# Performance work log

Measured on AMD Instinct MI355X. Metric: run time of the kernel, lower is better.

Reference implementation:

```python
import jax, jax.numpy as jnp
import numpy as np

V, E, G = 25000, 50000, 1024
D_IN, E_IN, D, EH = 74, 12, 64, 128
STEPS, S2S, L, NT = 6, 6, 3, 1


def setup_inputs() -> dict:
    key = jax.random.key(0)
    ks = jax.random.split(key, 20)
    p = lambda k, shp: (jax.random.normal(k, shp, jnp.float32) * 0.05)
    return {
        "node_feats": jax.random.normal(ks[0], (V, D_IN), jnp.float32),
        "edge_feats": jax.random.normal(ks[1], (E, E_IN), jnp.float32),
        "src": jax.random.randint(ks[2], (E,), 0, V),
        "dst": jax.random.randint(ks[3], (E,), 0, V),
        "node2graph": jnp.sort(jax.random.randint(ks[4], (V,), 0, G)),
        "W_proj": p(ks[5], (D_IN, D)), "b_proj": jnp.zeros((D,), jnp.float32),
        "W_e1": p(ks[6], (E_IN, EH)), "b_e1": jnp.zeros((EH,), jnp.float32),
        "W_e2": p(ks[7], (EH, D * D)), "b_e2": jnp.zeros((D * D,), jnp.float32),
        "b_conv": jnp.zeros((D,), jnp.float32),
        "gru_W_ih": p(ks[8], (3 * D, D)), "gru_W_hh": p(ks[9], (3 * D, D)),
        "gru_b_ih": jnp.zeros((3 * D,), jnp.float32), "gru_b_hh": jnp.zeros((3 * D,), jnp.float32),
        "lstm_W_ih0": p(ks[10], (4 * D, 2 * D)), "lstm_W_hh0": p(ks[11], (4 * D, D)),
        "lstm_b_ih0": jnp.zeros((4 * D,), jnp.float32), "lstm_b_hh0": jnp.zeros((4 * D,), jnp.float32),
        "lstm_W_ih_r": p(ks[12], (L - 1, 4 * D, D)), "lstm_W_hh_r": p(ks[13], (L - 1, 4 * D, D)),
        "lstm_b_ih_r": jnp.zeros((L - 1, 4 * D), jnp.float32), "lstm_b_hh_r": jnp.zeros((L - 1, 4 * D), jnp.float32),
        "W1": p(ks[14], (2 * D, D)), "b1": jnp.zeros((D,), jnp.float32),
        "bn_gamma": jnp.ones((D,), jnp.float32), "bn_beta": jnp.zeros((D,), jnp.float32),
        "bn_mean": jnp.zeros((D,), jnp.float32), "bn_var": jnp.ones((D,), jnp.float32),
        "W2": p(ks[15], (D, 4 * NT)), "b2": jnp.zeros((4 * NT,), jnp.float32),
    }


def reference(node_feats, edge_feats, src, dst, node2graph,
              W_proj, b_proj, W_e1, b_e1, W_e2, b_e2, b_conv,
              gru_W_ih, gru_W_hh, gru_b_ih, gru_b_hh,
              lstm_W_ih0, lstm_W_hh0, lstm_b_ih0, lstm_b_hh0,
              lstm_W_ih_r, lstm_W_hh_r, lstm_b_ih_r, lstm_b_hh_r,
              W1, b1, bn_gamma, bn_beta, bn_mean, bn_var, W2, b2):
    # --- MPNNGNN: project + ReLU, then NNConv(sum) + ReLU + GRU, x STEPS ---
    h = jax.nn.relu(node_feats @ W_proj + b_proj)                       # (V, D)
    # edge network: per-edge (D,D) mixing matrix (edge_feats constant across steps)
    We = (jax.nn.relu(edge_feats @ W_e1 + b_e1) @ W_e2 + b_e2).reshape(E, D, D)

    def mp_step(hh, _):
        m = jnp.einsum('ed,edo->eo', hh[src], We)                       # per-edge message
        agg = jax.ops.segment_sum(m, dst, num_segments=V) + b_conv      # NNConv sum + bias
        x = jax.nn.relu(agg)
        gi = x @ gru_W_ih.T + gru_b_ih                                  # GRU (torch gate order r,z,n)
        gh = hh @ gru_W_hh.T + gru_b_hh
        ir, iz, inn = jnp.split(gi, 3, axis=-1)
        hr, hz, hn = jnp.split(gh, 3, axis=-1)
        r = jax.nn.sigmoid(ir + hr)
        z = jax.nn.sigmoid(iz + hz)
        n = jnp.tanh(inn + r * hn)
        return (1.0 - z) * n + z * hh, None

    h, _ = jax.lax.scan(mp_step, h, None, length=STEPS)

    # --- Set2Set readout ---
    q_star = jnp.zeros((G, 2 * D), h.dtype)
    hs = jnp.zeros((L, G, D), h.dtype)
    cs = jnp.zeros((L, G, D), h.dtype)
    for _ in range(S2S):
        x = q_star
        nh, nc = [], []
        for l in range(L):                                              # stacked LSTM, seq len 1
            Wih = lstm_W_ih0 if l == 0 else lstm_W_ih_r[l - 1]
            Whh = lstm_W_hh0 if l == 0 else lstm_W_hh_r[l - 1]
            bih = lstm_b_ih0 if l == 0 else lstm_b_ih_r[l - 1]
            bhh = lstm_b_hh0 if l == 0 else lstm_b_hh_r[l - 1]
            gates = x @ Wih.T + bih + hs[l] @ Whh.T + bhh               # torch order i,f,g,o
            i, f, g, o = jnp.split(gates, 4, axis=-1)
            c = jax.nn.sigmoid(f) * cs[l] + jax.nn.sigmoid(i) * jnp.tanh(g)
            hc = jax.nn.sigmoid(o) * jnp.tanh(c)
            nh.append(hc); nc.append(c)
            x = hc
        hs, cs = jnp.stack(nh), jnp.stack(nc)
        q = x                                                           # (G, D)
        e = jnp.sum(h * q[node2graph], axis=-1)                         # (V,) attention logits
        emax = jax.lax.stop_gradient(jax.ops.segment_max(e, node2graph, num_segments=G))
        emax = jnp.where(jnp.isfinite(emax), emax, 0.0)
        ez = jnp.exp(e - emax[node2graph])                              # per-graph softmax
        denom = jax.ops.segment_sum(ez, node2graph, num_segments=G)
        alpha = ez / jnp.maximum(denom[node2graph], 1e-12)
        readout = jax.ops.segment_sum(h * alpha[:, None], node2graph, num_segments=G)
        q_star = jnp.concatenate([q, readout], axis=-1)                 # (G, 2D)

    # --- evidential head: Linear + ReLU + BatchNorm(eval) + Linear ---
    h1 = jax.nn.relu(q_star @ W1 + b1)
    hbn = bn_gamma * (h1 - bn_mean) * jax.lax.rsqrt(bn_var + 1e-5) + bn_beta
    out = hbn @ W2 + b2                                                 # (G, 4*NT)
    means, logl, loga, logb = jnp.split(out, 4, axis=1)
    MINV = 1e-6
    lam = jax.nn.softplus(logl) + MINV
    alp = jax.nn.softplus(loga) + MINV + 1.0
    bet = jax.nn.softplus(logb) + MINV
    return jnp.stack([means, lam, alp, bet], axis=2).reshape(out.shape)
```

## Files before the change

kernel.cpp:

```cpp
#include <hip/hip_runtime.h>
#include <stdint.h>

#define V_N 25000
#define E_N 50000
#define G_N 1024
#define DIN 74
#define EIN 12
#define NSTEPS 6
#define NS2S 6
#define MPAD 50048

typedef unsigned int u32;
typedef unsigned short u16;
typedef __attribute__((ext_vector_type(8))) short bf16x8v;
typedef __attribute__((ext_vector_type(4))) float f32x4v;

typedef __attribute__((address_space(3))) void lds_void;
typedef __attribute__((address_space(1))) void gbl_void;

__device__ __forceinline__ void gload_lds16(const void* g, void* l) {
  __builtin_amdgcn_global_load_lds((gbl_void*)g, (lds_void*)l, 16, 0, 0);
}

__device__ __forceinline__ u16 f2bf(float f) {
  u32 u = __float_as_uint(f);
  u = (u + 0x7fffu + ((u >> 16) & 1u)) >> 16;
  return (u16)u;
}
__device__ __forceinline__ u32 pack2bf(float lo, float hi) {
  return (u32)f2bf(lo) | ((u32)f2bf(hi) << 16);
}
__device__ __forceinline__ float bflo(u32 w){ return __uint_as_float(w << 16); }
__device__ __forceinline__ float bfhi(u32 w){ return __uint_as_float(w & 0xffff0000u); }
__device__ __forceinline__ float sigf(float x){ return 1.f/(1.f + expf(-x)); }
__device__ __forceinline__ float splusf(float x){ return fmaxf(x, 0.f) + log1pf(expf(-fabsf(x))); }

__global__ void prep_kernel(const float* gWih, const float* gWhh,
                            const float* lWih0, const float* lWhh0,
                            const float* lWihr, const float* lWhhr,
                            const float* We2,
                            float* gWihT, float* gWhhT,
                            u32* TW40, u32* TU40, u32* TW4r, u32* TU4r,
                            u16* WbT) {
  int idx = blockIdx.x * 256 + threadIdx.x;
  if (idx < 12288) { int d = idx / 192, r = idx % 192; gWihT[idx] = gWih[r*64 + d]; return; }
  idx -= 12288;
  if (idx < 12288) { int d = idx / 192, r = idx % 192; gWhhT[idx] = gWhh[r*64 + d]; return; }
  idx -= 12288;
  if (idx < 16384) { int q = idx >> 2, j = idx & 3; int k8 = q >> 8, r = q & 255;
                     TW40[idx] = pack2bf(lWih0[r*128 + k8*8 + 2*j], lWih0[r*128 + k8*8 + 2*j + 1]); return; }
  idx -= 16384;
  if (idx < 8192)  { int q = idx >> 2, j = idx & 3; int k8 = q >> 8, r = q & 255;
                     TU40[idx] = pack2bf(lWhh0[r*64 + k8*8 + 2*j], lWhh0[r*64 + k8*8 + 2*j + 1]); return; }
  idx -= 8192;
  if (idx < 16384) { int l = idx >> 13, rem = idx & 8191; int q = rem >> 2, j = rem & 3;
                     int k8 = q >> 8, r = q & 255;
                     TW4r[idx] = pack2bf(lWihr[l*16384 + r*64 + k8*8 + 2*j],
                                         lWihr[l*16384 + r*64 + k8*8 + 2*j + 1]); return; }
  idx -= 16384;
  if (idx < 16384) { int l = idx >> 13, rem = idx & 8191; int q = rem >> 2, j = rem & 3;
                     int k8 = q >> 8, r = q & 255;
                     TU4r[idx] = pack2bf(lWhhr[l*16384 + r*64 + k8*8 + 2*j],
                                         lWhhr[l*16384 + r*64 + k8*8 + 2*j + 1]); return; }
  idx -= 16384;
  { int n = idx / 128, k = idx % 128; WbT[idx] = f2bf(We2[k*4096 + n]); }
}

__global__ void proj_kernel(const float* nf, const float* Wp, const float* bp, float* h) {
  int v = blockIdx.x * 4 + (threadIdx.x >> 6);
  int o = threadIdx.x & 63;
  if (v >= V_N) return;
  float acc = bp[o];
  const float* row = nf + (size_t)v * DIN;
  #pragma unroll 2
  for (int d = 0; d < DIN; ++d) acc += row[d] * Wp[d*64 + o];
  h[(size_t)v*64 + o] = fmaxf(acc, 0.f);
}

__global__ void edgenet_kernel(const float* ef, const float* W1, const float* b1, u16* zb) {
  int e = blockIdx.x * 2 + (threadIdx.x >> 7);
  int k = threadIdx.x & 127;
  float acc = 0.f;
  if (e < E_N) {
    acc = b1[k];
    const float* row = ef + (size_t)e * EIN;
    #pragma unroll
    for (int i = 0; i < EIN; ++i) acc += row[i] * W1[i*128 + k];
    acc = fmaxf(acc, 0.f);
  }
  zb[(size_t)e*128 + k] = f2bf(acc);
}

__global__ __launch_bounds__(512) void fusedmsg_kernel(const u16* zb, const u16* WbT, const float* be2,
                                                       const float* h, const int* src, const int* dst,
                                                       float* agg) {
  __shared__ __align__(16) u16 As[16384];
  __shared__ __align__(16) u16 Bs[2][16384];
  __shared__ float hS[128][66];
  int t = threadIdx.x;
  int e0 = blockIdx.x * 128;

  for (int it = 0; it < 16; ++it) {
    int idx = it * 512 + t;
    int el = idx >> 6, d = idx & 63;
    int e = e0 + el;
    int sv = (e < E_N) ? src[e] : 0;
    hS[el][d] = h[(size_t)sv * 64 + d];
  }
  {
    const char* Ag = (const char*)(zb + (size_t)e0 * 128);
    char* Al = (char*)As;
    #pragma unroll
    for (int it = 0; it < 4; ++it) {
      int f = it * 512 + t;
      int r = f >> 4, s = f & 15;
      int gc = s ^ (r & 7);
      gload_lds16(Ag + r*256 + gc*16, Al + (size_t)(f & ~63) * 16);
    }
  }
  {
    const char* Bg = (const char*)WbT;
    char* Bl = (char*)Bs[0];
    #pragma unroll
    for (int it = 0; it < 4; ++it) {
      int f = it * 512 + t;
      int r = f >> 4, s = f & 15;
      int gc = s ^ (r & 7);
      gload_lds16(Bg + r*256 + gc*16, Bl + (size_t)(f & ~63) * 16);
    }
  }
  __syncthreads();

  int w = t >> 6, lane = t & 63;
  int wr = w >> 1, wc = w & 1;
  float macc[2][4][4];
  #pragma unroll
  for (int mi = 0; mi < 2; ++mi)
    #pragma unroll
    for (int ni = 0; ni < 4; ++ni)
      #pragma unroll
      for (int r = 0; r < 4; ++r) macc[mi][ni][r] = 0.f;

  for (int nt = 0; nt < 32; ++nt) {
    int buf = nt & 1;
    if (nt < 31) {
      const char* Bg = (const char*)(WbT + (size_t)(nt + 1) * 128 * 128);
      char* Bl = (char*)Bs[buf ^ 1];
      #pragma unroll
      for (int it = 0; it < 4; ++it) {
        int f = it * 512 + t;
        int r = f >> 4, s = f & 15;
        int gc = s ^ (r & 7);
        gload_lds16(Bg + r*256 + gc*16, Bl + (size_t)(f & ~63) * 16);
      }
    }
    f32x4v acc[2][4];
    #pragma unroll
    for (int ni = 0; ni < 4; ++ni) {
      float b = be2[nt*128 + wc*64 + ni*16 + (lane & 15)];
      #pragma unroll
      for (int mi = 0; mi < 2; ++mi) acc[mi][ni] = (f32x4v){b, b, b, b};
    }
    const char* Ab = (const char*)As;
    const char* Bb = (const char*)Bs[buf];
    #pragma unroll
    for (int ks = 0; ks < 4; ++ks) {
      int cb = ks * 4 + (lane >> 4);
      bf16x8v af[2], bf[4];
      #pragma unroll
      for (int mi = 0; mi < 2; ++mi) {
        int arow = wr*32 + mi*16 + (lane & 15);
        af[mi] = *(const bf16x8v*)(Ab + arow*256 + ((cb ^ (arow & 7)) << 4));
      }
      #pragma unroll
      for (int ni = 0; ni < 4; ++ni) {
        int brow = wc*64 + ni*16 + (lane & 15);
        bf[ni] = *(const bf16x8v*)(Bb + brow*256 + ((cb ^ (brow & 7)) << 4));
      }
      #pragma unroll
      for (int mi = 0; mi < 2; ++mi)
        #pragma unroll
        for (int ni = 0; ni < 4; ++ni)
          acc[mi][ni] = __builtin_amdgcn_mfma_f32_16x16x32_bf16(af[mi], bf[ni], acc[mi][ni], 0, 0, 0);
    }
    int d0 = 2*nt + wc;
    #pragma unroll
    for (int mi = 0; mi < 2; ++mi)
      #pragma unroll
      for (int r = 0; r < 4; ++r) {
        int row = wr*32 + mi*16 + ((lane >> 4) << 2) + r;
        float hv = hS[row][d0];
        #pragma unroll
        for (int ni = 0; ni < 4; ++ni)
          macc[mi][ni][r] += hv * acc[mi][ni][r];
      }
    __syncthreads();
  }

  float* red = (float*)Bs;
  __syncthreads();
  if (wc == 1) {
    #pragma unroll
    for (int mi = 0; mi < 2; ++mi)
      #pragma unroll
      for (int ni = 0; ni < 4; ++ni)
        #pragma unroll
        for (int r = 0; r < 4; ++r)
          red[((wr*64 + lane)*32) + (mi*4 + ni)*4 + r] = macc[mi][ni][r];
  }
  __syncthreads();
  if (wc == 0) {
    #pragma unroll
    for (int mi = 0; mi < 2; ++mi)
      #pragma unroll
      for (int r = 0; r < 4; ++r) {
        int row = wr*32 + mi*16 + ((lane >> 4) << 2) + r;
        int e = e0 + row;
        if (e < E_N) {
          int dv = dst[e];
          #pragma unroll
          for (int ni = 0; ni < 4; ++ni) {
            float val = macc[mi][ni][r] + red[((wr*64 + lane)*32) + (mi*4 + ni)*4 + r];
            atomicAdd(&agg[(size_t)dv*64 + ni*16 + (lane & 15)], val);
          }
        }
      }
  }
}

__global__ void gru_kernel(const float* aggc, const float* bconv, const float* WihT, const float* WhhT,
                           const float* bih, const float* bhh, float* h, float* aggz) {
  int wbase = (blockIdx.x * 4 + (threadIdx.x >> 6)) * 4;
  int o = threadIdx.x & 63;
  float xv[4], hv[4];
  #pragma unroll
  for (int n = 0; n < 4; ++n) {
    int v = wbase + n;
    if (v < V_N) { xv[n] = fmaxf(aggc[(size_t)v*64 + o] + bconv[o], 0.f); hv[n] = h[(size_t)v*64 + o]; }
    else { xv[n] = 0.f; hv[n] = 0.f; }
  }
  float ar[4] = {0,0,0,0}, az[4] = {0,0,0,0}, an[4] = {0,0,0,0};
  float br[4] = {0,0,0,0}, bz[4] = {0,0,0,0}, bn2[4] = {0,0,0,0};
  #pragma unroll 4
  for (int d = 0; d < 64; ++d) {
    float wr = WihT[d*192 + o], wz = WihT[d*192 + 64 + o], wn = WihT[d*192 + 128 + o];
    float ur = WhhT[d*192 + o], uz = WhhT[d*192 + 64 + o], un = WhhT[d*192 + 128 + o];
    #pragma unroll
    for (int n = 0; n < 4; ++n) {
      float xd = __shfl(xv[n], d);
      float hd = __shfl(hv[n], d);
      ar[n] += xd*wr; az[n] += xd*wz; an[n] += xd*wn;
      br[n] += hd*ur; bz[n] += hd*uz; bn2[n] += hd*un;
    }
  }
  float b_r = bih[o] + bhh[o], b_z = bih[64+o] + bhh[64+o];
  float bin = bih[128+o], bhn = bhh[128+o];
  #pragma unroll
  for (int n = 0; n < 4; ++n) {
    int v = wbase + n;
    if (v >= V_N) continue;
    float r  = sigf(ar[n] + br[n] + b_r);
    float z  = sigf(az[n] + bz[n] + b_z);
    float nn = tanhf(an[n] + bin + r*(bn2[n] + bhn));
    h[(size_t)v*64 + o] = (1.f - z)*nn + z*hv[n];
    aggz[(size_t)v*64 + o] = 0.f;
  }
}

__global__ void gstart_kernel(const int* n2g, int* gstart) {
  int g = blockIdx.x * 256 + threadIdx.x;
  if (g > G_N) return;
  int lo = 0, hi = V_N;
  while (lo < hi) { int mid = (lo + hi) >> 1; if (n2g[mid] < g) lo = mid + 1; else hi = mid; }
  gstart[g] = lo;
}

__global__ __launch_bounds__(256) void s2s_kernel(const float* h, const int* gstart,
    const uint4* TW40, const uint4* TU40, const uint4* TW4r, const uint4* TU4r,
    const float* bih0, const float* bhh0, const float* bihr, const float* bhhr,
    float* qstar) {
  __shared__ float sq[4][128];
  __shared__ float sx[4][128];
  __shared__ float shs[4][3][64], scs[4][3][64];
  __shared__ float sg[4][256];
  int tt = threadIdx.x;
  int g0blk = blockIdx.x * 4;
  int w = tt >> 6, lane = tt & 63;
  int nstart = gstart[g0blk + w], nend = gstart[g0blk + w + 1];

  for (int i = tt; i < 512; i += 256) ((float*)sq)[i] = 0.f;
  for (int i = tt; i < 768; i += 256) { ((float*)shs)[i] = 0.f; ((float*)scs)[i] = 0.f; }
  __syncthreads();

  for (int iter = 0; iter < NS2S; ++iter) {
    for (int i = tt; i < 512; i += 256) ((float*)sx)[i] = ((float*)sq)[i];
    __syncthreads();

    for (int l = 0; l < 3; ++l) {
      const uint4* TW = (l == 0) ? TW40 : TW4r + (size_t)(l-1) * 2048;
      const uint4* TU = (l == 0) ? TU40 : TU4r + (size_t)(l-1) * 2048;
      const float* bi = (l == 0) ? bih0 : bihr + (l-1)*256;
      const float* bh = (l == 0) ? bhh0 : bhhr + (l-1)*256;
      float bsum = bi[tt] + bh[tt];
      float acc[4] = {bsum, bsum, bsum, bsum};
      if (l == 0) {
        #pragma unroll
        for (int k8 = 0; k8 < 16; ++k8) {
          uint4 u = TW[k8*256 + tt];
          #pragma unroll
          for (int gi = 0; gi < 4; ++gi) {
            const float4 xa = *(const float4*)&sx[gi][k8*8];
            const float4 xb = *(const float4*)&sx[gi][k8*8 + 4];
            acc[gi] += xa.x*bflo(u.x) + xa.y*bfhi(u.x) + xa.z*bflo(u.y) + xa.w*bfhi(u.y)
                     + xb.x*bflo(u.z) + xb.y*bfhi(u.z) + xb.z*bflo(u.w) + xb.w*bfhi(u.w);
          }
        }
      } else {
        #pragma unroll
        for (int k8 = 0; k8 < 8; ++k8) {
          uint4 u = TW[k8*256 + tt];
          #pragma unroll
          for (int gi = 0; gi < 4; ++gi) {
            const float4 xa = *(const float4*)&sx[gi][k8*8];
            const float4 xb = *(const float4*)&sx[gi][k8*8 + 4];
            acc[gi] += xa.x*bflo(u.x) + xa.y*bfhi(u.x) + xa.z*bflo(u.y) + xa.w*bfhi(u.y)
                     + xb.x*bflo(u.z) + xb.y*bfhi(u.z) + xb.z*bflo(u.w) + xb.w*bfhi(u.w);
          }
        }
      }
      #pragma unroll
      for (int k8 = 0; k8 < 8; ++k8) {
        uint4 u = TU[k8*256 + tt];
        #pragma unroll
        for (int gi = 0; gi < 4; ++gi) {
          const float4 ha = *(const float4*)&shs[gi][l][k8*8];
          const float4 hb = *(const float4*)&shs[gi][l][k8*8 + 4];
          acc[gi] += ha.x*bflo(u.x) + ha.y*bfhi(u.x) + ha.z*bflo(u.y) + ha.w*bfhi(u.y)
                   + hb.x*bflo(u.z) + hb.y*bfhi(u.z) + hb.z*bflo(u.w) + hb.w*bfhi(u.w);
        }
      }
      #pragma unroll
      for (int gi = 0; gi < 4; ++gi) sg[gi][tt] = acc[gi];
      __syncthreads();
      {
        int gq = tt >> 6, r = tt & 63;
        float gv_i = sg[gq][r], gv_f = sg[gq][64+r], gv_g = sg[gq][128+r], gv_o = sg[gq][192+r];
        float c = sigf(gv_f)*scs[gq][l][r] + sigf(gv_i)*tanhf(gv_g);
        float hc = sigf(gv_o)*tanhf(c);
        scs[gq][l][r] = c; shs[gq][l][r] = hc; sx[gq][r] = hc;
      }
      __syncthreads();
    }

    {
      float q_l = sx[w][lane];
      float lmax = -3.4e38f;
      int i = nstart;
      for (; i + 1 < nend; i += 2) {
        float h0 = h[(size_t)i*64 + lane];
        float h1 = h[(size_t)(i+1)*64 + lane];
        float v0 = h0 * q_l, v1 = h1 * q_l;
        #pragma unroll
        for (int off = 32; off; off >>= 1) { v0 += __shfl_xor(v0, off); v1 += __shfl_xor(v1, off); }
        lmax = fmaxf(lmax, fmaxf(v0, v1));
      }
      if (i < nend) {
        float h0 = h[(size_t)i*64 + lane];
        float v0 = h0 * q_l;
        #pragma unroll
        for (int off = 32; off; off >>= 1) v0 += __shfl_xor(v0, off);
        lmax = fmaxf(lmax, v0);
      }
      float lsum = 0.f, accv = 0.f;
      i = nstart;
      for (; i + 1 < nend; i += 2) {
        float h0 = h[(size_t)i*64 + lane];
        float h1 = h[(size_t)(i+1)*64 + lane];
        float v0 = h0 * q_l, v1 = h1 * q_l;
        #pragma unroll
        for (int off = 32; off; off >>= 1) { v0 += __shfl_xor(v0, off); v1 += __shfl_xor(v1, off); }
        float e0 = expf(v0 - lmax), e1 = expf(v1 - lmax);
        lsum += e0 + e1; accv += e0*h0 + e1*h1;
      }
      if (i < nend) {
        float h0 = h[(size_t)i*64 + lane];
        float v0 = h0 * q_l;
        #pragma unroll
        for (int off = 32; off; off >>= 1) v0 += __shfl_xor(v0, off);
        float e0 = expf(v0 - lmax);
        lsum += e0; accv += e0*h0;
      }
      sq[w][lane] = sx[w][lane];
      sq[w][64 + lane] = accv / fmaxf(lsum, 1e-12f);
    }
    __syncthreads();
  }

  for (int i = tt; i < 512; i += 256) qstar[(size_t)g0blk * 128 + i] = ((float*)sq)[i];
}

__global__ void head_kernel(const float* qstar, const float* W1, const float* b1,
                            const float* gma, const float* gbe, const float* gme, const float* gva,
                            const float* W2, const float* b2, float* out) {
  __shared__ float hb[4][64];
  int wslot = threadIdx.x >> 6;
  int g = blockIdx.x * 4 + wslot;
  int o = threadIdx.x & 63;
  float acc = b1[o];
  const float* q = qstar + (size_t)g * 128;
  #pragma unroll 4
  for (int k = 0; k < 128; ++k) acc += q[k] * W1[k*64 + o];
  acc = fmaxf(acc, 0.f);
  float hbn = gma[o] * (acc - gme[o]) * rsqrtf(gva[o] + 1e-5f) + gbe[o];
  hb[wslot][o] = hbn;
  __syncthreads();
  if (o < 4) {
    float v = b2[o];
    #pragma unroll 8
    for (int k = 0; k < 64; ++k) v += hb[wslot][k] * W2[k*4 + o];
    float res;
    if (o == 0) res = v;
    else { res = splusf(v) + 1e-6f; if (o == 2) res += 1.f; }
    out[(size_t)g*4 + o] = res;
  }
}

extern "C" void kernel_launch(void* const* d_in, const int* in_sizes, int n_in,
                              void* d_out, int out_size, void* d_ws, size_t ws_size,
                              hipStream_t stream) {
  const float* node_feats = (const float*)d_in[0];
  const float* edge_feats = (const float*)d_in[1];
  const int*   src        = (const int*)d_in[2];
  const int*   dst        = (const int*)d_in[3];
  const int*   n2g        = (const int*)d_in[4];
  const float* W_proj = (const float*)d_in[5];
  const float* b_proj = (const float*)d_in[6];
  const float* W_e1   = (const float*)d_in[7];
  const float* b_e1   = (const float*)d_in[8];
  const float* W_e2   = (const float*)d_in[9];
  const float* b_e2   = (const float*)d_in[10];
  const float* b_conv = (const float*)d_in[11];
  const float* gru_W_ih = (const float*)d_in[12];
  const float* gru_W_hh = (const float*)d_in[13];
  const float* gru_b_ih = (const float*)d_in[14];
  const float* gru_b_hh = (const float*)d_in[15];
  const float* lstm_W_ih0 = (const float*)d_in[16];
  const float* lstm_W_hh0 = (const float*)d_in[17];
  const float* lstm_b_ih0 = (const float*)d_in[18];
  const float* lstm_b_hh0 = (const float*)d_in[19];
  const float* lstm_W_ih_r = (const float*)d_in[20];
  const float* lstm_W_hh_r = (const float*)d_in[21];
  const float* lstm_b_ih_r = (const float*)d_in[22];
  const float* lstm_b_hh_r = (const float*)d_in[23];
  const float* W1 = (const float*)d_in[24];
  const float* b1 = (const float*)d_in[25];
  const float* bn_gamma = (const float*)d_in[26];
  const float* bn_beta  = (const float*)d_in[27];
  const float* bn_mean  = (const float*)d_in[28];
  const float* bn_var   = (const float*)d_in[29];
  const float* W2 = (const float*)d_in[30];
  const float* b2 = (const float*)d_in[31];

  char* ws = (char*)d_ws;
  size_t off = 0;
  auto alloc = [&](size_t n) { size_t c = off; off += (n + 255) & ~(size_t)255; return c; };
  u16*   zb     = (u16*)  (ws + alloc((size_t)MPAD * 128 * 2));
  float* h      = (float*)(ws + alloc((size_t)V_N * 64 * 4));
  float* agg    = (float*)(ws + alloc((size_t)V_N * 64 * 4));
  u16*   WbT    = (u16*)  (ws + alloc((size_t)4096 * 128 * 2));
  float* gWihT  = (float*)(ws + alloc(12288 * 4));
  float* gWhhT  = (float*)(ws + alloc(12288 * 4));
  u32*   TW40   = (u32*)  (ws + alloc(16384 * 4));
  u32*   TU40   = (u32*)  (ws + alloc(8192 * 4));
  u32*   TW4r   = (u32*)  (ws + alloc(16384 * 4));
  u32*   TU4r   = (u32*)  (ws + alloc(16384 * 4));
  int*   gstart = (int*)  (ws + alloc(1025 * 4));
  float* qstar  = (float*)(ws + alloc((size_t)G_N * 128 * 4));
  (void)in_sizes; (void)n_in; (void)out_size; (void)ws_size;

  prep_kernel<<<2368, 256, 0, stream>>>(gru_W_ih, gru_W_hh, lstm_W_ih0, lstm_W_hh0,
                                        lstm_W_ih_r, lstm_W_hh_r, W_e2,
                                        gWihT, gWhhT, TW40, TU40, TW4r, TU4r, WbT);
  proj_kernel<<<6250, 256, 0, stream>>>(node_feats, W_proj, b_proj, h);
  edgenet_kernel<<<MPAD / 2, 256, 0, stream>>>(edge_feats, W_e1, b_e1, zb);
  hipMemsetAsync(agg, 0, (size_t)V_N * 64 * 4, stream);

  for (int st = 0; st < NSTEPS; ++st) {
    fusedmsg_kernel<<<MPAD / 128, 512, 0, stream>>>(zb, WbT, b_e2, h, src, dst, agg);
    gru_kernel<<<1563, 256, 0, stream>>>(agg, b_conv, gWihT, gWhhT, gru_b_ih, gru_b_hh, h, agg);
  }

  gstart_kernel<<<5, 256, 0, stream>>>(n2g, gstart);
  s2s_kernel<<<256, 256, 0, stream>>>(h, gstart, (const uint4*)TW40, (const uint4*)TU40,
                                      (const uint4*)TW4r, (const uint4*)TU4r,
                                      lstm_b_ih0, lstm_b_hh0, lstm_b_ih_r, lstm_b_hh_r, qstar);
  head_kernel<<<256, 256, 0, stream>>>(qstar, W1, b1, bn_gamma, bn_beta, bn_mean, bn_var,
                                       W2, b2, (float*)d_out);
}
```

Baseline: 1.227 ms.

## Rewrite fused message kernel as single-wave blocks with register-resident A and global B

```diff
diff --git a/kernel.cpp b/kernel.cpp
--- a/kernel.cpp
+++ b/kernel.cpp
@@ -14,13 +14,6 @@
 typedef unsigned short u16;
 typedef __attribute__((ext_vector_type(8))) short bf16x8v;
 typedef __attribute__((ext_vector_type(4))) float f32x4v;
-
-typedef __attribute__((address_space(3))) void lds_void;
-typedef __attribute__((address_space(1))) void gbl_void;
-
-__device__ __forceinline__ void gload_lds16(const void* g, void* l) {
-  __builtin_amdgcn_global_load_lds((gbl_void*)g, (lds_void*)l, 16, 0, 0);
-}
 
 __device__ __forceinline__ u16 f2bf(float f) {
   u32 u = __float_as_uint(f);
@@ -91,141 +84,83 @@
   zb[(size_t)e*128 + k] = f2bf(acc);
 }
 
-__global__ __launch_bounds__(512) void fusedmsg_kernel(const u16* zb, const u16* WbT, const float* be2,
-                                                       const float* h, const int* src, const int* dst,
-                                                       float* agg) {
-  __shared__ __align__(16) u16 As[16384];
-  __shared__ __align__(16) u16 Bs[2][16384];
-  __shared__ float hS[128][66];
-  int t = threadIdx.x;
-  int e0 = blockIdx.x * 128;
-
-  for (int it = 0; it < 16; ++it) {
-    int idx = it * 512 + t;
-    int el = idx >> 6, d = idx & 63;
-    int e = e0 + el;
+__global__ __launch_bounds__(64) void fusedmsg_kernel(const u16* zb, const u16* WbT, const float* be2,
+                                                      const float* h, const int* src, const int* dst,
+                                                      float* agg) {
+  __shared__ float hS[64][65];
+  int lane = threadIdx.x;
+  int e0 = blockIdx.x * 64;
+  int l16 = lane & 15, lh = lane >> 4;
+
+  for (int row = 0; row < 64; ++row) {
+    int e = e0 + row;
     int sv = (e < E_N) ? src[e] : 0;
-    hS[el][d] = h[(size_t)sv * 64 + d];
-  }
-  {
-    const char* Ag = (const char*)(zb + (size_t)e0 * 128);
-    char* Al = (char*)As;
-    #pragma unroll
-    for (int it = 0; it < 4; ++it) {
-      int f = it * 512 + t;
-      int r = f >> 4, s = f & 15;
-      int gc = s ^ (r & 7);
-      gload_lds16(Ag + r*256 + gc*16, Al + (size_t)(f & ~63) * 16);
+    hS[row][lane] = h[(size_t)sv * 64 + lane];
+  }
+
+  bf16x8v af[4][4];
+  #pragma unroll
+  for (int rf = 0; rf < 4; ++rf)
+    #pragma unroll
+    for (int ks = 0; ks < 4; ++ks)
+      af[rf][ks] = *(const bf16x8v*)(zb + (size_t)(e0 + rf*16 + l16)*128 + ks*32 + lh*8);
+
+  f32x4v m[4][4];
+  #pragma unroll
+  for (int rf = 0; rf < 4; ++rf)
+    #pragma unroll
+    for (int of = 0; of < 4; ++of)
+      #pragma unroll
+      for (int r = 0; r < 4; ++r) m[rf][of][r] = 0.f;
+
+  #pragma unroll 2
+  for (int d = 0; d < 64; ++d) {
+    float hv[4][4];
+    #pragma unroll
+    for (int rf = 0; rf < 4; ++rf)
+      #pragma unroll
+      for (int r = 0; r < 4; ++r)
+        hv[rf][r] = hS[rf*16 + lh*4 + r][d];
+
+    #pragma unroll
+    for (int of = 0; of < 4; ++of) {
+      const u16* Bb = WbT + (size_t)(d*64 + of*16 + l16)*128 + lh*8;
+      bf16x8v b0 = *(const bf16x8v*)(Bb);
+      bf16x8v b1 = *(const bf16x8v*)(Bb + 32);
+      bf16x8v b2 = *(const bf16x8v*)(Bb + 64);
+      bf16x8v b3 = *(const bf16x8v*)(Bb + 96);
+      float bias = be2[d*64 + of*16 + l16];
+      f32x4v c[4];
+      #pragma unroll
+      for (int rf = 0; rf < 4; ++rf) c[rf] = (f32x4v){bias, bias, bias, bias};
+      #pragma unroll
+      for (int rf = 0; rf < 4; ++rf) {
+        c[rf] = __builtin_amdgcn_mfma_f32_16x16x32_bf16(af[rf][0], b0, c[rf], 0, 0, 0);
+        c[rf] = __builtin_amdgcn_mfma_f32_16x16x32_bf16(af[rf][1], b1, c[rf], 0, 0, 0);
+        c[rf] = __builtin_amdgcn_mfma_f32_16x16x32_bf16(af[rf][2], b2, c[rf], 0, 0, 0);
+        c[rf] = __builtin_amdgcn_mfma_f32_16x16x32_bf16(af[rf][3], b3, c[rf], 0, 0, 0);
+      }
+      #pragma unroll
+      for (int rf = 0; rf < 4; ++rf)
+        #pragma unroll
+        for (int r = 0; r < 4; ++r)
+          m[rf][of][r] += hv[rf][r] * c[rf][r];
     }
   }
-  {
-    const char* Bg = (const char*)WbT;
-    char* Bl = (char*)Bs[0];
-    #pragma unroll
-    for (int it = 0; it < 4; ++it) {
-      int f = it * 512 + t;
-      int r = f >> 4, s = f & 15;
-      int gc = s ^ (r & 7);
-      gload_lds16(Bg + r*256 + gc*16, Bl + (size_t)(f & ~63) * 16);
+
+  #pragma unroll
+  for (int rf = 0; rf < 4; ++rf)
+    #pragma unroll
+    for (int r = 0; r < 4; ++r) {
+      int row = rf*16 + lh*4 + r;
+      int e = e0 + row;
+      if (e < E_N) {
+        int dv = dst[e];
+        #pragma unroll
+        for (int of = 0; of < 4; ++of)
+          atomicAdd(&agg[(size_t)dv*64 + of*16 + l16], m[rf][of][r]);
+      }
     }
-  }
-  __syncthreads();
-
-  int w = t >> 6, lane = t & 63;
-  int wr = w >> 1, wc = w & 1;
-  float macc[2][4][4];
-  #pragma unroll
-  for (int mi = 0; mi < 2; ++mi)
-    #pragma unroll
-    for (int ni = 0; ni < 4; ++ni)
-      #pragma unroll
-      for (int r = 0; r < 4; ++r) macc[mi][ni][r] = 0.f;
-
-  for (int nt = 0; nt < 32; ++nt) {
-    int buf = nt & 1;
-    if (nt < 31) {
-      const char* Bg = (const char*)(WbT + (size_t)(nt + 1) * 128 * 128);
-      char* Bl = (char*)Bs[buf ^ 1];
-      #pragma unroll
-      for (int it = 0; it < 4; ++it) {
-        int f = it * 512 + t;
-        int r = f >> 4, s = f & 15;
-        int gc = s ^ (r & 7);
-        gload_lds16(Bg + r*256 + gc*16, Bl + (size_t)(f & ~63) * 16);
-      }
-    }
-    f32x4v acc[2][4];
-    #pragma unroll
-    for (int ni = 0; ni < 4; ++ni) {
-      float b = be2[nt*128 + wc*64 + ni*16 + (lane & 15)];
-      #pragma unroll
-      for (int mi = 0; mi < 2; ++mi) acc[mi][ni] = (f32x4v){b, b, b, b};
-    }
-    const char* Ab = (const char*)As;
-    const char* Bb = (const char*)Bs[buf];
-    #pragma unroll
-    for (int ks = 0; ks < 4; ++ks) {
-      int cb = ks * 4 + (lane >> 4);
-      bf16x8v af[2], bf[4];
-      #pragma unroll
-      for (int mi = 0; mi < 2; ++mi) {
-        int arow = wr*32 + mi*16 + (lane & 15);
-        af[mi] = *(const bf16x8v*)(Ab + arow*256 + ((cb ^ (arow & 7)) << 4));
-      }
-      #pragma unroll
-      for (int ni = 0; ni < 4; ++ni) {
-        int brow = wc*64 + ni*16 + (lane & 15);
-        bf[ni] = *(const bf16x8v*)(Bb + brow*256 + ((cb ^ (brow & 7)) << 4));
-      }
-      #pragma unroll
-      for (int mi = 0; mi < 2; ++mi)
-        #pragma unroll
-        for (int ni = 0; ni < 4; ++ni)
-          acc[mi][ni] = __builtin_amdgcn_mfma_f32_16x16x32_bf16(af[mi], bf[ni], acc[mi][ni], 0, 0, 0);
-    }
-    int d0 = 2*nt + wc;
-    #pragma unroll
-    for (int mi = 0; mi < 2; ++mi)
-      #pragma unroll
-      for (int r = 0; r < 4; ++r) {
-        int row = wr*32 + mi*16 + ((lane >> 4) << 2) + r;
-        float hv = hS[row][d0];
-        #pragma unroll
-        for (int ni = 0; ni < 4; ++ni)
-          macc[mi][ni][r] += hv * acc[mi][ni][r];
-      }
-    __syncthreads();
-  }
-
-  float* red = (float*)Bs;
-  __syncthreads();
-  if (wc == 1) {
-    #pragma unroll
-    for (int mi = 0; mi < 2; ++mi)
-      #pragma unroll
-      for (int ni = 0; ni < 4; ++ni)
-        #pragma unroll
-        for (int r = 0; r < 4; ++r)
-          red[((wr*64 + lane)*32) + (mi*4 + ni)*4 + r] = macc[mi][ni][r];
-  }
-  __syncthreads();
-  if (wc == 0) {
-    #pragma unroll
-    for (int mi = 0; mi < 2; ++mi)
-      #pragma unroll
-      for (int r = 0; r < 4; ++r) {
-        int row = wr*32 + mi*16 + ((lane >> 4) << 2) + r;
-        int e = e0 + row;
-        if (e < E_N) {
-          int dv = dst[e];
-          #pragma unroll
-          for (int ni = 0; ni < 4; ++ni) {
-            float val = macc[mi][ni][r] + red[((wr*64 + lane)*32) + (mi*4 + ni)*4 + r];
-            atomicAdd(&agg[(size_t)dv*64 + ni*16 + (lane & 15)], val);
-          }
-        }
-      }
-  }
 }
 
 __global__ void gru_kernel(const float* aggc, const float* bconv, const float* WihT, const float* WhhT,
@@ -486,7 +421,7 @@
   hipMemsetAsync(agg, 0, (size_t)V_N * 64 * 4, stream);
 
   for (int st = 0; st < NSTEPS; ++st) {
-    fusedmsg_kernel<<<MPAD / 128, 512, 0, stream>>>(zb, WbT, b_e2, h, src, dst, agg);
+    fusedmsg_kernel<<<MPAD / 64, 64, 0, stream>>>(zb, WbT, b_e2, h, src, dst, agg);
     gru_kernel<<<1563, 256, 0, stream>>>(agg, b_conv, gWihT, gWhhT, gru_b_ih, gru_b_hh, h, agg);
   }
 
```

After: 1.555 ms. +26.7%, slower.
